# Kernel optimization log

Measured on AMD Instinct MI355X. Metric: run time of the kernel, lower is better.

## Reference

```python
import jax, jax.numpy as jnp
import numpy as np

DIM = 4194304
EPS = 1e-24


def setup_inputs() -> dict:
    key = jax.random.key(0)
    ks = jax.random.split(key, 17)
    dim = DIM
    s = 0.3  # weight scale ~ kaiming for small fan-in
    inp = {
        "gradient": jax.random.normal(ks[0], (dim,), jnp.float32),
        "x_prev": jax.random.normal(ks[1], (dim,), jnp.float32),
        "x_curr": jax.random.normal(ks[2], (dim,), jnp.float32),
        "loss_curr": jax.random.uniform(ks[3], (1,), jnp.float32),
        "loss_prev": jax.random.uniform(ks[4], (1,), jnp.float32),
        "Wc1": s * jax.random.normal(ks[5], (10, 3), jnp.float32),
        "Wc2": s * jax.random.normal(ks[6], (10, 10), jnp.float32),
        "Wc3": s * jax.random.normal(ks[7], (10, 10), jnp.float32),
        "Wc4": s * jax.random.normal(ks[8], (10, 10), jnp.float32),
        "Wc5": s * jax.random.normal(ks[9], (10, 10), jnp.float32),
        "Wc6": s * jax.random.normal(ks[10], (10, 10), jnp.float32),
        "Wc7": s * jax.random.normal(ks[11], (1, 10), jnp.float32),
        "Wl1": s * jax.random.normal(ks[12], (8, 4), jnp.float32),
        "Wl2": s * jax.random.normal(ks[13], (8, 8), jnp.float32),
        "Wl3": s * jax.random.normal(ks[14], (8, 8), jnp.float32),
        "Wl4": s * jax.random.normal(ks[15], (8, 8), jnp.float32),
        "Wl5": s * jax.random.normal(ks[16], (1, 8), jnp.float32),
    }
    return inp


def reference(gradient, x_prev, x_curr, loss_curr, loss_prev,
              Wc1, Wc2, Wc3, Wc4, Wc5, Wc6, Wc7,
              Wl1, Wl2, Wl3, Wl4, Wl5):
    relu = jax.nn.relu

    g_norm = jnp.linalg.norm(gradient)
    g = jnp.where(g_norm > EPS, gradient / g_norm, gradient)

    momentum = x_curr - x_prev
    m_norm = jnp.linalg.norm(momentum)
    m = jnp.where(m_norm > EPS, momentum / m_norm, momentum)

    # coefficients MLP on log(1 + scalar features); losses are detached in torch
    feats = jnp.log1p(jnp.stack([
        g_norm,
        m_norm,
        jax.lax.stop_gradient(loss_curr[0]),
        jax.lax.stop_gradient(loss_prev[0]),
    ]))  # [4]
    h = relu(Wl1 @ feats)
    h = relu(Wl2 @ h)
    h = relu(Wl3 @ h)
    h = Wl4 @ h
    step_size = Wl5 @ h  # [1]

    # direction network: 1x1 convs over the parameter dimension -> channel matmuls
    x = jnp.stack([g, m, g * m], axis=0)  # [3, dim]
    d = Wc1 @ x          # conv1 (no activation)
    d = Wc2 @ d          # conv2
    d = relu(d)
    d = relu(Wc3 @ d)
    d = relu(Wc4 @ d)
    d = relu(Wc5 @ d)
    d = Wc6 @ d          # conv6 (no activation)
    d = Wc7 @ d          # conv7 -> [1, dim]
    direction = d.reshape(-1)  # [dim]

    return x_curr - step_size * direction
```

## Files before the change

kernel.cpp:

```cpp
#include <hip/hip_runtime.h>
#include <math.h>
#include <stdint.h>

#define DIM 4194304
#define RBLOCKS 1024
#define RTHREADS 256
#define FBLOCKS 2048
#define FTHREADS 256
#define TOTTH (FBLOCKS * FTHREADS)
#define PASSES (DIM / TOTTH)
#define EPSF 1e-24f
#define SCALE 256.0f

#define WS_PART 0
#define WS_W21 2048
#define WS_W3 2176
#define WS_W4 2304
#define WS_W5 2432
#define WS_W67 2560

typedef uint32_t u32;
typedef __fp16 fp16x2 __attribute__((ext_vector_type(2)));
typedef __fp16 half8 __attribute__((ext_vector_type(8)));
typedef float f32x4 __attribute__((ext_vector_type(4)));
typedef uint32_t u32x2 __attribute__((ext_vector_type(2)));
typedef uint32_t u32x4 __attribute__((ext_vector_type(4)));

__device__ __forceinline__ u32 pack2u(float a, float b) {
    fp16x2 r = __builtin_amdgcn_cvt_pkrtz(a, b);
    return __builtin_bit_cast(u32, r);
}

__device__ __forceinline__ f32x4 mfma32(half8 a, half8 b, f32x4 c) {
    return __builtin_amdgcn_mfma_f32_16x16x32_f16(a, b, c, 0, 0, 0);
}
__device__ __forceinline__ half8 relucvt8(f32x4 a) {
    fp16x2 z2 = {(__fp16)0.f, (__fp16)0.f};
    fp16x2 c0 = __builtin_amdgcn_cvt_pkrtz(a[0], a[1]);
    fp16x2 c1 = __builtin_amdgcn_cvt_pkrtz(a[2], a[3]);
    c0 = __builtin_elementwise_max(c0, z2);
    c1 = __builtin_elementwise_max(c1, z2);
    u32x4 r = {__builtin_bit_cast(u32, c0), __builtin_bit_cast(u32, c1), 0u, 0u};
    return __builtin_bit_cast(half8, r);
}

__global__ __launch_bounds__(RTHREADS) void k_reduce(
    const float* __restrict__ grad, const float* __restrict__ xp, const float* __restrict__ xc,
    const float* __restrict__ Wc1, const float* __restrict__ Wc2, const float* __restrict__ Wc3,
    const float* __restrict__ Wc4, const float* __restrict__ Wc5, const float* __restrict__ Wc6,
    const float* __restrict__ Wc7, float* __restrict__ ws) {
    if (blockIdx.x == 0) {
        u32* wsu = (u32*)ws;
        int t = threadIdx.x;
        if (t < 128) {
            int lane = t >> 1, d = t & 1;
            int m = lane & 15, gg = lane >> 4;
            int k0 = 4 * gg + 2 * d;
            float a0 = 0.f, a1 = 0.f;
            if (m < 10 && k0 < 3) {
                for (int j = 0; j < 10; ++j) a0 += Wc2[m * 10 + j] * Wc1[j * 3 + k0];
                if (k0 == 2) a0 *= (1.f / SCALE);
            }
            if (m < 10 && k0 + 1 < 3) {
                for (int j = 0; j < 10; ++j) a1 += Wc2[m * 10 + j] * Wc1[j * 3 + k0 + 1];
                if (k0 + 1 == 2) a1 *= (1.f / SCALE);
            }
            wsu[WS_W21 + t] = pack2u(a0, a1);
            float v0, v1;
            v0 = (m < 10 && k0 < 10) ? Wc3[m * 10 + k0] : 0.f;
            v1 = (m < 10 && k0 + 1 < 10) ? Wc3[m * 10 + k0 + 1] : 0.f;
            wsu[WS_W3 + t] = pack2u(v0, v1);
            v0 = (m < 10 && k0 < 10) ? Wc4[m * 10 + k0] : 0.f;
            v1 = (m < 10 && k0 + 1 < 10) ? Wc4[m * 10 + k0 + 1] : 0.f;
            wsu[WS_W4 + t] = pack2u(v0, v1);
            v0 = (m < 10 && k0 < 10) ? Wc5[m * 10 + k0] : 0.f;
            v1 = (m < 10 && k0 + 1 < 10) ? Wc5[m * 10 + k0 + 1] : 0.f;
            wsu[WS_W5 + t] = pack2u(v0, v1);
        }
        if (t >= 128 && t < 144) {
            int j = t - 128;
            float w = 0.f;
            if (j < 10)
                for (int k = 0; k < 10; ++k) w += Wc7[k] * Wc6[k * 10 + j];
            ws[WS_W67 + j] = w;
        }
    }
    const float4* g4 = reinterpret_cast<const float4*>(grad);
    const float4* p4 = reinterpret_cast<const float4*>(xp);
    const float4* c4 = reinterpret_cast<const float4*>(xc);
    int tid = blockIdx.x * RTHREADS + threadIdx.x;
    float sg = 0.f, sm = 0.f;
    constexpr int STRIDE = RBLOCKS * RTHREADS;
#pragma unroll
    for (int it = 0; it < (DIM / 4) / STRIDE; ++it) {
        int i = tid + it * STRIDE;
        float4 gv = g4[i];
        float4 pv = p4[i];
        float4 cv = c4[i];
        sg += gv.x * gv.x + gv.y * gv.y + gv.z * gv.z + gv.w * gv.w;
        float mx = cv.x - pv.x, my = cv.y - pv.y, mz = cv.z - pv.z, mw = cv.w - pv.w;
        sm += mx * mx + my * my + mz * mz + mw * mw;
    }
#pragma unroll
    for (int off = 32; off > 0; off >>= 1) {
        sg += __shfl_down(sg, off);
        sm += __shfl_down(sm, off);
    }
    __shared__ float wg[4], wm[4];
    int wave = threadIdx.x >> 6;
    if ((threadIdx.x & 63) == 0) {
        wg[wave] = sg;
        wm[wave] = sm;
    }
    __syncthreads();
    if (threadIdx.x == 0) {
        ws[WS_PART + 2 * blockIdx.x]     = wg[0] + wg[1] + wg[2] + wg[3];
        ws[WS_PART + 2 * blockIdx.x + 1] = wm[0] + wm[1] + wm[2] + wm[3];
    }
}

__global__ __launch_bounds__(FTHREADS, 8) void k_fused(
    const float* __restrict__ grad, const float* __restrict__ xp, const float* __restrict__ xc,
    const float* __restrict__ loss_curr, const float* __restrict__ loss_prev,
    const float* __restrict__ Wl1, const float* __restrict__ Wl2, const float* __restrict__ Wl3,
    const float* __restrict__ Wl4, const float* __restrict__ Wl5,
    const float* __restrict__ ws, float* __restrict__ out) {
    __shared__ float sc[3];
    __shared__ float red[8];
    const int tid = threadIdx.x;
    const int lane = tid & 63;

    {
        float fg = 0.f, fm = 0.f;
        for (int i = tid; i < RBLOCKS; i += FTHREADS) {
            fg += ws[WS_PART + 2 * i];
            fm += ws[WS_PART + 2 * i + 1];
        }
#pragma unroll
        for (int off = 32; off > 0; off >>= 1) {
            fg += __shfl_down(fg, off);
            fm += __shfl_down(fm, off);
        }
        int wv = tid >> 6;
        if ((tid & 63) == 0) {
            red[wv] = fg;
            red[4 + wv] = fm;
        }
        __syncthreads();
        if (tid < 64) {
            float g2 = red[0] + red[1] + red[2] + red[3];
            float m2 = red[4] + red[5] + red[6] + red[7];
            float g_norm = sqrtf(g2), m_norm = sqrtf(m2);
            float g_inv = (g_norm > EPSF) ? 1.f / g_norm : 1.f;
            float m_inv = (m_norm > EPSF) ? 1.f / m_norm : 1.f;
            float f0 = log1pf(g_norm), f1 = log1pf(m_norm);
            float f2 = log1pf(loss_curr[0]), f3 = log1pf(loss_prev[0]);
            int o = tid & 7;
            float h = fmaxf(Wl1[o * 4] * f0 + Wl1[o * 4 + 1] * f1 + Wl1[o * 4 + 2] * f2 +
                                Wl1[o * 4 + 3] * f3,
                            0.f);
            float acc = 0.f;
#pragma unroll
            for (int i = 0; i < 8; ++i) acc += Wl2[o * 8 + i] * __shfl(h, i);
            h = fmaxf(acc, 0.f);
            acc = 0.f;
#pragma unroll
            for (int i = 0; i < 8; ++i) acc += Wl3[o * 8 + i] * __shfl(h, i);
            h = fmaxf(acc, 0.f);
            acc = 0.f;
#pragma unroll
            for (int i = 0; i < 8; ++i) acc += Wl4[o * 8 + i] * __shfl(h, i);
            h = acc;
            float step = 0.f;
#pragma unroll
            for (int i = 0; i < 8; ++i) step += Wl5[i] * __shfl(h, i);
            if (tid == 0) {
                sc[0] = g_inv * SCALE;
                sc[1] = m_inv * SCALE;
                sc[2] = step * (1.f / SCALE);
            }
        }
        __syncthreads();
    }
    const float gs = sc[0], ms = sc[1], step_eff = sc[2];

    const u32* wsu = (const u32*)ws;
    const int n = lane & 15, g = lane >> 4;
#define LOADFRAG(NAME, OFS)                                                    \
    half8 NAME;                                                                \
    {                                                                          \
        u32x2 lo = ((const u32x2*)(wsu + (OFS)))[lane];                        \
        u32x4 fr = {lo[0], lo[1], 0u, 0u};                                     \
        NAME = __builtin_bit_cast(half8, fr);                                  \
    }
    LOADFRAG(w21f, WS_W21)
    LOADFRAG(w3f, WS_W3)
    LOADFRAG(w4f, WS_W4)
    LOADFRAG(w5f, WS_W5)
#undef LOADFRAG
    half8 w67f;
    {
        const float* w67p = ws + WS_W67;
        u32x4 fr = {pack2u(w67p[4 * g], w67p[4 * g + 1]),
                    pack2u(w67p[4 * g + 2], w67p[4 * g + 3]), 0u, 0u};
        w67f = __builtin_bit_cast(half8, fr);
    }
    const f32x4 zf = {0.f, 0.f, 0.f, 0.f};

    int ebase = (blockIdx.x * (FTHREADS / 64) + (tid >> 6)) * 64 + lane;
    int e = ebase;
    float gvv = grad[e], pvv = xp[e], cvv = xc[e];
#pragma unroll
    for (int p = 0; p < PASSES; ++p) {
        int en = (p + 1 < PASSES) ? (e + TOTTH) : 0;
        float gvn = grad[en], pvn = xp[en], cvn = xc[en];

        float Gf = gvv * gs;
        float Mf = (cvv - pvv) * ms;
        float GMf = Gf * Mf;
        u32 pk0 = pack2u(Gf, Mf), pk1 = pack2u(GMf, 0.f);

        float dhalf0, dhalf1;
#pragma unroll
        for (int st = 0; st < 2; ++st) {
            u32 b0[2], b1[2];
#pragma unroll
            for (int t = 0; t < 2; ++t) {
                int idx = (n + 16 * (2 * st + t)) << 2;
                b0[t] = (u32)__builtin_amdgcn_ds_bpermute(idx, (int)pk0);
                b1[t] = (u32)__builtin_amdgcn_ds_bpermute(idx, (int)pk1);
            }
            f32x4 acc[2];
#pragma unroll
            for (int t = 0; t < 2; ++t) {
                u32x4 bb = {b0[t], b1[t], 0u, 0u};
                acc[t] = mfma32(w21f, __builtin_bit_cast(half8, bb), zf);
            }
#pragma unroll
            for (int t = 0; t < 2; ++t) acc[t] = mfma32(w3f, relucvt8(acc[t]), zf);
#pragma unroll
            for (int t = 0; t < 2; ++t) acc[t] = mfma32(w4f, relucvt8(acc[t]), zf);
#pragma unroll
            for (int t = 0; t < 2; ++t) acc[t] = mfma32(w5f, relucvt8(acc[t]), zf);
#pragma unroll
            for (int t = 0; t < 2; ++t) acc[t] = mfma32(w67f, relucvt8(acc[t]), zf);
            float dsel = ((g & 1) == 0) ? acc[0][0] : acc[1][0];
            if (st == 0)
                dhalf0 = dsel;
            else
                dhalf1 = dsel;
        }
        float dsel = (g < 2) ? dhalf0 : dhalf1;
        out[e] = fmaf(-step_eff, dsel, cvv);

        e = (p + 1 < PASSES) ? en : e;
        gvv = gvn;
        pvv = pvn;
        cvv = cvn;
    }
}

extern "C" void kernel_launch(void* const* d_in, const int* in_sizes, int n_in,
                              void* d_out, int out_size, void* d_ws, size_t ws_size,
                              hipStream_t stream) {
    const float* grad      = (const float*)d_in[0];
    const float* xp        = (const float*)d_in[1];
    const float* xc        = (const float*)d_in[2];
    const float* loss_curr = (const float*)d_in[3];
    const float* loss_prev = (const float*)d_in[4];
    const float* Wc1 = (const float*)d_in[5];
    const float* Wc2 = (const float*)d_in[6];
    const float* Wc3 = (const float*)d_in[7];
    const float* Wc4 = (const float*)d_in[8];
    const float* Wc5 = (const float*)d_in[9];
    const float* Wc6 = (const float*)d_in[10];
    const float* Wc7 = (const float*)d_in[11];
    const float* Wl1 = (const float*)d_in[12];
    const float* Wl2 = (const float*)d_in[13];
    const float* Wl3 = (const float*)d_in[14];
    const float* Wl4 = (const float*)d_in[15];
    const float* Wl5 = (const float*)d_in[16];

    float* ws  = (float*)d_ws;
    float* out = (float*)d_out;

    k_reduce<<<RBLOCKS, RTHREADS, 0, stream>>>(grad, xp, xc, Wc1, Wc2, Wc3, Wc4, Wc5, Wc6,
                                               Wc7, ws);
    k_fused<<<FBLOCKS, FTHREADS, 0, stream>>>(grad, xp, xc, loss_curr, loss_prev, Wl1, Wl2,
                                              Wl3, Wl4, Wl5, ws, out);
}
```

Before: 38.88 us.

## Split scalar MLP into single-wave kernel and deepen input prefetch to two passes

Result: slower. 42.60 us (+9.6%).

```diff
diff --git a/kernel.cpp b/kernel.cpp
--- a/kernel.cpp
+++ b/kernel.cpp
@@ -18,6 +18,7 @@
 #define WS_W4 2304
 #define WS_W5 2432
 #define WS_W67 2560
+#define WS_SC 2576
 
 typedef uint32_t u32;
 typedef __fp16 fp16x2 __attribute__((ext_vector_type(2)));
@@ -119,70 +120,65 @@
     }
 }
 
-__global__ __launch_bounds__(FTHREADS, 8) void k_fused(
-    const float* __restrict__ grad, const float* __restrict__ xp, const float* __restrict__ xc,
-    const float* __restrict__ loss_curr, const float* __restrict__ loss_prev,
-    const float* __restrict__ Wl1, const float* __restrict__ Wl2, const float* __restrict__ Wl3,
-    const float* __restrict__ Wl4, const float* __restrict__ Wl5,
-    const float* __restrict__ ws, float* __restrict__ out) {
-    __shared__ float sc[3];
-    __shared__ float red[8];
+__global__ __launch_bounds__(64) void k_scalar(const float* __restrict__ loss_curr,
+                                               const float* __restrict__ loss_prev,
+                                               const float* __restrict__ Wl1,
+                                               const float* __restrict__ Wl2,
+                                               const float* __restrict__ Wl3,
+                                               const float* __restrict__ Wl4,
+                                               const float* __restrict__ Wl5,
+                                               float* __restrict__ ws) {
+    int lane = threadIdx.x;
+    float fg = 0.f, fm = 0.f;
+    for (int i = lane; i < RBLOCKS; i += 64) {
+        fg += ws[WS_PART + 2 * i];
+        fm += ws[WS_PART + 2 * i + 1];
+    }
+#pragma unroll
+    for (int off = 32; off > 0; off >>= 1) {
+        fg += __shfl_down(fg, off);
+        fm += __shfl_down(fm, off);
+    }
+    float g2 = __shfl(fg, 0), m2 = __shfl(fm, 0);
+    float g_norm = sqrtf(g2), m_norm = sqrtf(m2);
+    float g_inv = (g_norm > EPSF) ? 1.f / g_norm : 1.f;
+    float m_inv = (m_norm > EPSF) ? 1.f / m_norm : 1.f;
+    float f0 = log1pf(g_norm), f1 = log1pf(m_norm);
+    float f2 = log1pf(loss_curr[0]), f3 = log1pf(loss_prev[0]);
+    int o = lane & 7;
+    float h = fmaxf(Wl1[o * 4] * f0 + Wl1[o * 4 + 1] * f1 + Wl1[o * 4 + 2] * f2 +
+                        Wl1[o * 4 + 3] * f3,
+                    0.f);
+    float acc = 0.f;
+#pragma unroll
+    for (int i = 0; i < 8; ++i) acc += Wl2[o * 8 + i] * __shfl(h, i);
+    h = fmaxf(acc, 0.f);
+    acc = 0.f;
+#pragma unroll
+    for (int i = 0; i < 8; ++i) acc += Wl3[o * 8 + i] * __shfl(h, i);
+    h = fmaxf(acc, 0.f);
+    acc = 0.f;
+#pragma unroll
+    for (int i = 0; i < 8; ++i) acc += Wl4[o * 8 + i] * __shfl(h, i);
+    h = acc;
+    float step = 0.f;
+#pragma unroll
+    for (int i = 0; i < 8; ++i) step += Wl5[i] * __shfl(h, i);
+    if (lane == 0) {
+        ws[WS_SC + 0] = g_inv * SCALE;
+        ws[WS_SC + 1] = m_inv * SCALE;
+        ws[WS_SC + 2] = step * (1.f / SCALE);
+    }
+}
+
+__global__ __launch_bounds__(FTHREADS, 8) void k_net(const float* __restrict__ grad,
+                                                     const float* __restrict__ xp,
+                                                     const float* __restrict__ xc,
+                                                     const float* __restrict__ ws,
+                                                     float* __restrict__ out) {
     const int tid = threadIdx.x;
     const int lane = tid & 63;
-
-    {
-        float fg = 0.f, fm = 0.f;
-        for (int i = tid; i < RBLOCKS; i += FTHREADS) {
-            fg += ws[WS_PART + 2 * i];
-            fm += ws[WS_PART + 2 * i + 1];
-        }
-#pragma unroll
-        for (int off = 32; off > 0; off >>= 1) {
-            fg += __shfl_down(fg, off);
-            fm += __shfl_down(fm, off);
-        }
-        int wv = tid >> 6;
-        if ((tid & 63) == 0) {
-            red[wv] = fg;
-            red[4 + wv] = fm;
-        }
-        __syncthreads();
-        if (tid < 64) {
-            float g2 = red[0] + red[1] + red[2] + red[3];
-            float m2 = red[4] + red[5] + red[6] + red[7];
-            float g_norm = sqrtf(g2), m_norm = sqrtf(m2);
-            float g_inv = (g_norm > EPSF) ? 1.f / g_norm : 1.f;
-            float m_inv = (m_norm > EPSF) ? 1.f / m_norm : 1.f;
-            float f0 = log1pf(g_norm), f1 = log1pf(m_norm);
-            float f2 = log1pf(loss_curr[0]), f3 = log1pf(loss_prev[0]);
-            int o = tid & 7;
-            float h = fmaxf(Wl1[o * 4] * f0 + Wl1[o * 4 + 1] * f1 + Wl1[o * 4 + 2] * f2 +
-                                Wl1[o * 4 + 3] * f3,
-                            0.f);
-            float acc = 0.f;
-#pragma unroll
-            for (int i = 0; i < 8; ++i) acc += Wl2[o * 8 + i] * __shfl(h, i);
-            h = fmaxf(acc, 0.f);
-            acc = 0.f;
-#pragma unroll
-            for (int i = 0; i < 8; ++i) acc += Wl3[o * 8 + i] * __shfl(h, i);
-            h = fmaxf(acc, 0.f);
-            acc = 0.f;
-#pragma unroll
-            for (int i = 0; i < 8; ++i) acc += Wl4[o * 8 + i] * __shfl(h, i);
-            h = acc;
-            float step = 0.f;
-#pragma unroll
-            for (int i = 0; i < 8; ++i) step += Wl5[i] * __shfl(h, i);
-            if (tid == 0) {
-                sc[0] = g_inv * SCALE;
-                sc[1] = m_inv * SCALE;
-                sc[2] = step * (1.f / SCALE);
-            }
-        }
-        __syncthreads();
-    }
-    const float gs = sc[0], ms = sc[1], step_eff = sc[2];
+    const float gs = ws[WS_SC + 0], ms = ws[WS_SC + 1], step_eff = ws[WS_SC + 2];
 
     const u32* wsu = (const u32*)ws;
     const int n = lane & 15, g = lane >> 4;
@@ -207,13 +203,26 @@
     }
     const f32x4 zf = {0.f, 0.f, 0.f, 0.f};
 
-    int ebase = (blockIdx.x * (FTHREADS / 64) + (tid >> 6)) * 64 + lane;
-    int e = ebase;
-    float gvv = grad[e], pvv = xp[e], cvv = xc[e];
+    const int ebase = (blockIdx.x * (FTHREADS / 64) + (tid >> 6)) * 64 + lane;
+
+    float gbuf[2], pbuf[2], cbuf[2];
+    gbuf[0] = grad[ebase];
+    pbuf[0] = xp[ebase];
+    cbuf[0] = xc[ebase];
+    gbuf[1] = grad[ebase + TOTTH];
+    pbuf[1] = xp[ebase + TOTTH];
+    cbuf[1] = xc[ebase + TOTTH];
+
 #pragma unroll
     for (int p = 0; p < PASSES; ++p) {
-        int en = (p + 1 < PASSES) ? (e + TOTTH) : 0;
-        float gvn = grad[en], pvn = xp[en], cvn = xc[en];
+        const int slot = p & 1;
+        float gvv = gbuf[slot], pvv = pbuf[slot], cvv = cbuf[slot];
+        if (p + 2 < PASSES) {
+            int ei = ebase + (p + 2) * TOTTH;
+            gbuf[slot] = grad[ei];
+            pbuf[slot] = xp[ei];
+            cbuf[slot] = xc[ei];
+        }
 
         float Gf = gvv * gs;
         float Mf = (cvv - pvv) * ms;
@@ -251,12 +260,7 @@
                 dhalf1 = dsel;
         }
         float dsel = (g < 2) ? dhalf0 : dhalf1;
-        out[e] = fmaf(-step_eff, dsel, cvv);
-
-        e = (p + 1 < PASSES) ? en : e;
-        gvv = gvn;
-        pvv = pvn;
-        cvv = cvn;
+        out[ebase + p * TOTTH] = fmaf(-step_eff, dsel, cvv);
     }
 }
 
@@ -286,6 +290,6 @@
 
     k_reduce<<<RBLOCKS, RTHREADS, 0, stream>>>(grad, xp, xc, Wc1, Wc2, Wc3, Wc4, Wc5, Wc6,
                                                Wc7, ws);
-    k_fused<<<FBLOCKS, FTHREADS, 0, stream>>>(grad, xp, xc, loss_curr, loss_prev, Wl1, Wl2,
-                                              Wl3, Wl4, Wl5, ws, out);
-}
+    k_scalar<<<1, 64, 0, stream>>>(loss_curr, loss_prev, Wl1, Wl2, Wl3, Wl4, Wl5, ws);
+    k_net<<<FBLOCKS, FTHREADS, 0, stream>>>(grad, xp, xc, ws, out);
+}
```

## Stash packed fp16 gradient/momentum in reduce pass and reuse in fused pass

Applied to the files above, without the earlier changes.

Result: slower. 41.42 us (+6.6%).

```diff
diff --git a/kernel.cpp b/kernel.cpp
--- a/kernel.cpp
+++ b/kernel.cpp
@@ -7,8 +7,8 @@
 #define RTHREADS 256
 #define FBLOCKS 2048
 #define FTHREADS 256
-#define TOTTH (FBLOCKS * FTHREADS)
-#define PASSES (DIM / TOTTH)
+#define NWAVES (FBLOCKS * FTHREADS / 64)
+#define PASSES (DIM / 64 / NWAVES)
 #define EPSF 1e-24f
 #define SCALE 256.0f
 
@@ -18,6 +18,7 @@
 #define WS_W4 2304
 #define WS_W5 2432
 #define WS_W67 2560
+#define WS_GM 4096
 
 typedef uint32_t u32;
 typedef __fp16 fp16x2 __attribute__((ext_vector_type(2)));
@@ -28,6 +29,10 @@
 
 __device__ __forceinline__ u32 pack2u(float a, float b) {
     fp16x2 r = __builtin_amdgcn_cvt_pkrtz(a, b);
+    return __builtin_bit_cast(u32, r);
+}
+__device__ __forceinline__ u32 pkmul(u32 a, u32 b) {
+    fp16x2 r = __builtin_bit_cast(fp16x2, a) * __builtin_bit_cast(fp16x2, b);
     return __builtin_bit_cast(u32, r);
 }
 
@@ -49,8 +54,8 @@
     const float* __restrict__ Wc1, const float* __restrict__ Wc2, const float* __restrict__ Wc3,
     const float* __restrict__ Wc4, const float* __restrict__ Wc5, const float* __restrict__ Wc6,
     const float* __restrict__ Wc7, float* __restrict__ ws) {
+    u32* wsu = (u32*)ws;
     if (blockIdx.x == 0) {
-        u32* wsu = (u32*)ws;
         int t = threadIdx.x;
         if (t < 128) {
             int lane = t >> 1, d = t & 1;
@@ -88,6 +93,7 @@
     const float4* g4 = reinterpret_cast<const float4*>(grad);
     const float4* p4 = reinterpret_cast<const float4*>(xp);
     const float4* c4 = reinterpret_cast<const float4*>(xc);
+    u32x4* gm4 = reinterpret_cast<u32x4*>(wsu + WS_GM);
     int tid = blockIdx.x * RTHREADS + threadIdx.x;
     float sg = 0.f, sm = 0.f;
     constexpr int STRIDE = RBLOCKS * RTHREADS;
@@ -97,9 +103,11 @@
         float4 gv = g4[i];
         float4 pv = p4[i];
         float4 cv = c4[i];
+        float mx = cv.x - pv.x, my = cv.y - pv.y, mz = cv.z - pv.z, mw = cv.w - pv.w;
         sg += gv.x * gv.x + gv.y * gv.y + gv.z * gv.z + gv.w * gv.w;
-        float mx = cv.x - pv.x, my = cv.y - pv.y, mz = cv.z - pv.z, mw = cv.w - pv.w;
         sm += mx * mx + my * my + mz * mz + mw * mw;
+        u32x4 gm = {pack2u(gv.x, mx), pack2u(gv.y, my), pack2u(gv.z, mz), pack2u(gv.w, mw)};
+        gm4[i] = gm;
     }
 #pragma unroll
     for (int off = 32; off > 0; off >>= 1) {
@@ -120,12 +128,13 @@
 }
 
 __global__ __launch_bounds__(FTHREADS, 8) void k_fused(
-    const float* __restrict__ grad, const float* __restrict__ xp, const float* __restrict__ xc,
-    const float* __restrict__ loss_curr, const float* __restrict__ loss_prev,
-    const float* __restrict__ Wl1, const float* __restrict__ Wl2, const float* __restrict__ Wl3,
+    const float* __restrict__ xc, const float* __restrict__ loss_curr,
+    const float* __restrict__ loss_prev, const float* __restrict__ Wl1,
+    const float* __restrict__ Wl2, const float* __restrict__ Wl3,
     const float* __restrict__ Wl4, const float* __restrict__ Wl5,
     const float* __restrict__ ws, float* __restrict__ out) {
-    __shared__ float sc[3];
+    __shared__ float sc_step;
+    __shared__ u32 sc_hs;
     __shared__ float red[8];
     const int tid = threadIdx.x;
     const int lane = tid & 63;
@@ -175,14 +184,14 @@
 #pragma unroll
             for (int i = 0; i < 8; ++i) step += Wl5[i] * __shfl(h, i);
             if (tid == 0) {
-                sc[0] = g_inv * SCALE;
-                sc[1] = m_inv * SCALE;
-                sc[2] = step * (1.f / SCALE);
+                sc_step = step * (1.f / SCALE);
+                sc_hs = pack2u(g_inv * SCALE, m_inv * SCALE);
             }
         }
         __syncthreads();
     }
-    const float gs = sc[0], ms = sc[1], step_eff = sc[2];
+    const float step_eff = sc_step;
+    const u32 hs = sc_hs;
 
     const u32* wsu = (const u32*)ws;
     const int n = lane & 15, g = lane >> 4;
@@ -206,35 +215,35 @@
         w67f = __builtin_bit_cast(half8, fr);
     }
     const f32x4 zf = {0.f, 0.f, 0.f, 0.f};
-
-    int ebase = (blockIdx.x * (FTHREADS / 64) + (tid >> 6)) * 64 + lane;
-    int e = ebase;
-    float gvv = grad[e], pvv = xp[e], cvv = xc[e];
+    const u32* gmu = wsu + WS_GM;
+    const int wave_gid = blockIdx.x * (FTHREADS / 64) + (tid >> 6);
+
 #pragma unroll
     for (int p = 0; p < PASSES; ++p) {
-        int en = (p + 1 < PASSES) ? (e + TOTTH) : 0;
-        float gvn = grad[en], pvn = xp[en], cvn = xc[en];
-
-        float Gf = gvv * gs;
-        float Mf = (cvv - pvv) * ms;
-        float GMf = Gf * Mf;
-        u32 pk0 = pack2u(Gf, Mf), pk1 = pack2u(GMf, 0.f);
+        const int grp = wave_gid + p * NWAVES;
+        const int e = grp * 64 + lane;
+        float cvv = xc[e];
+
+        u32 raw0 = gmu[grp * 64 + n];
+        u32 raw1 = gmu[grp * 64 + n + 16];
+        u32 raw2 = gmu[grp * 64 + n + 32];
+        u32 raw3 = gmu[grp * 64 + n + 48];
 
         float dhalf0, dhalf1;
 #pragma unroll
         for (int st = 0; st < 2; ++st) {
-            u32 b0[2], b1[2];
-#pragma unroll
-            for (int t = 0; t < 2; ++t) {
-                int idx = (n + 16 * (2 * st + t)) << 2;
-                b0[t] = (u32)__builtin_amdgcn_ds_bpermute(idx, (int)pk0);
-                b1[t] = (u32)__builtin_amdgcn_ds_bpermute(idx, (int)pk1);
-            }
+            u32 ra = (st == 0) ? raw0 : raw2;
+            u32 rb = (st == 0) ? raw1 : raw3;
+            u32 pk0a = pkmul(ra, hs);
+            u32 pk0b = pkmul(rb, hs);
+            u32 pk1a = pkmul(pk0a, (pk0a >> 16) | (pk0a << 16));
+            u32 pk1b = pkmul(pk0b, (pk0b >> 16) | (pk0b << 16));
             f32x4 acc[2];
-#pragma unroll
-            for (int t = 0; t < 2; ++t) {
-                u32x4 bb = {b0[t], b1[t], 0u, 0u};
-                acc[t] = mfma32(w21f, __builtin_bit_cast(half8, bb), zf);
+            {
+                u32x4 ba = {pk0a, pk1a, 0u, 0u};
+                u32x4 bb = {pk0b, pk1b, 0u, 0u};
+                acc[0] = mfma32(w21f, __builtin_bit_cast(half8, ba), zf);
+                acc[1] = mfma32(w21f, __builtin_bit_cast(half8, bb), zf);
             }
 #pragma unroll
             for (int t = 0; t < 2; ++t) acc[t] = mfma32(w3f, relucvt8(acc[t]), zf);
@@ -252,11 +261,6 @@
         }
         float dsel = (g < 2) ? dhalf0 : dhalf1;
         out[e] = fmaf(-step_eff, dsel, cvv);
-
-        e = (p + 1 < PASSES) ? en : e;
-        gvv = gvn;
-        pvv = pvn;
-        cvv = cvn;
     }
 }
 
@@ -286,6 +290,6 @@
 
     k_reduce<<<RBLOCKS, RTHREADS, 0, stream>>>(grad, xp, xc, Wc1, Wc2, Wc3, Wc4, Wc5, Wc6,
                                                Wc7, ws);
-    k_fused<<<FBLOCKS, FTHREADS, 0, stream>>>(grad, xp, xc, loss_curr, loss_prev, Wl1, Wl2,
-                                              Wl3, Wl4, Wl5, ws, out);
-}
+    k_fused<<<FBLOCKS, FTHREADS, 0, stream>>>(xc, loss_curr, loss_prev, Wl1, Wl2, Wl3, Wl4,
+                                              Wl5, ws, out);
+}
```
